# Performance work log

Measured on AMD Instinct MI355X. Metric: run time of the kernel, lower is better.

## Reference

```python
import jax, jax.numpy as jnp
import numpy as np

N_NODES = 100000
N_PART = 5000
N_EDGES = 1000000
D_NODE = 128
D_PART = 128
D_ATT = 20


def setup_inputs() -> dict:
    key = jax.random.key(0)
    ks = jax.random.split(key, 20)
    inp = {
        "nodes_hidden": jax.random.normal(ks[0], (N_NODES, D_NODE), jnp.float32),
        "particles_hidden": jax.random.normal(ks[1], (N_PART, D_PART), jnp.float32),
        "global_rep": jax.random.normal(ks[2], (N_PART, D_NODE), jnp.float32),
        "src": jax.random.randint(ks[3], (N_EDGES,), 0, N_NODES, jnp.int32),
        "dst": jax.random.randint(ks[4], (N_EDGES,), 0, N_PART, jnp.int32),
        "key_W": jax.random.normal(ks[5], (D_NODE, D_ATT), jnp.float32) * 0.05,
        "key_b": jnp.zeros((D_ATT,), jnp.float32),
        "val_W": jax.random.normal(ks[6], (D_NODE, D_PART), jnp.float32) * 0.05,
        "val_b": jnp.zeros((D_PART,), jnp.float32),
        "q_W": jax.random.normal(ks[7], (D_PART + D_NODE, D_ATT), jnp.float32) * 0.05,
        "q_b": jnp.zeros((D_ATT,), jnp.float32),
        "W_ih": jax.random.normal(ks[8], (3 * D_PART, D_PART), jnp.float32) * 0.05,
        "W_hh": jax.random.normal(ks[9], (3 * D_PART, D_PART), jnp.float32) * 0.05,
        "b_ih": jnp.zeros((3 * D_PART,), jnp.float32),
        "b_hh": jnp.zeros((3 * D_PART,), jnp.float32),
        "ln_g": jnp.ones((D_PART,), jnp.float32),
        "ln_b": jnp.zeros((D_PART,), jnp.float32),
        "mlp_W1": jax.random.normal(ks[10], (D_PART, 64), jnp.float32) * 0.05,
        "mlp_b1": jnp.zeros((64,), jnp.float32),
        "mlp_W2": jax.random.normal(ks[11], (64, D_PART), jnp.float32) * 0.05,
        "mlp_b2": jnp.zeros((D_PART,), jnp.float32),
    }
    return inp


def reference(nodes_hidden, particles_hidden, global_rep, src, dst,
              key_W, key_b, val_W, val_b, q_W, q_b,
              W_ih, W_hh, b_ih, b_hh, ln_g, ln_b,
              mlp_W1, mlp_b1, mlp_W2, mlp_b2):
    norm = jnp.float32(1.0) / jnp.sqrt(jnp.float32(D_ATT))
    keys = nodes_hidden @ key_W + key_b          # [N, 20]
    vals = nodes_hidden @ val_W + val_b          # [N, P]
    q_in = jnp.concatenate([particles_hidden, global_rep], axis=1)
    query = q_in @ q_W + q_b                     # [Np, 20]

    # per-edge raw attention (ReLU'd copy in edges.data is unused downstream)
    att = jnp.sum(keys[src] * query[dst], axis=1) * norm     # [E]
    msg = att[:, None] * vals[src]                            # [E, P]
    weighted_sum = jax.ops.segment_sum(msg, dst, num_segments=particles_hidden.shape[0])

    # GRUCell(input=weighted_sum, hidden=particles_hidden), torch semantics
    gi = weighted_sum @ W_ih.T + b_ih
    gh = particles_hidden @ W_hh.T + b_hh
    i_r, i_z, i_n = jnp.split(gi, 3, axis=1)
    h_r, h_z, h_n = jnp.split(gh, 3, axis=1)
    r = jax.nn.sigmoid(i_r + h_r)
    z = jax.nn.sigmoid(i_z + h_z)
    n = jnp.tanh(i_n + r * h_n)
    h_new = (1.0 - z) * n + z * particles_hidden

    # LayerNorm (eps=1e-5)
    mu = jnp.mean(h_new, axis=-1, keepdims=True)
    var = jnp.mean(jnp.square(h_new - mu), axis=-1, keepdims=True)
    ln = (h_new - mu) * jax.lax.rsqrt(var + 1e-5) * ln_g + ln_b

    mlp_out = jax.nn.relu(ln @ mlp_W1 + mlp_b1) @ mlp_W2 + mlp_b2
    return particles_hidden + mlp_out
```

## Files before the change

kernel.cpp:

```cpp
#include <hip/hip_runtime.h>
#include <math.h>

#define N_NODES 100000
#define N_PART  5000
#define N_EDGES 1000000
#define D_NODE  128
#define D_PART  128
#define D_ATT   20
#define NBLK    128
#define EPB     ((N_EDGES + NBLK - 1) / NBLK)
#define TPV6    8

__device__ __forceinline__ float sigmoid_(float x) { return 1.f / (1.f + __expf(-x)); }
__device__ __forceinline__ float tanh_(float x)    { return 1.f - 2.f / (__expf(2.f * x) + 1.f); }

__global__ __launch_bounds__(256) void build_wbig_kernel(
    const float* __restrict__ valW, const float* __restrict__ Wih,
    const float* __restrict__ Whh, float* __restrict__ Wbig)
{
    int idx = blockIdx.x * 256 + threadIdx.x;
    int k = idx >> 9;
    int jn = idx & 511;
    int j = (jn & 3) * 128 + (jn >> 2);
    float v = 0.f;
    if (k < 128) {
        if (j < 384) {
            float acc = 0.f;
            #pragma unroll 8
            for (int m = 0; m < 128; m++)
                acc += valW[k * 128 + m] * Wih[j * 128 + m];
            v = acc;
        }
    } else {
        int kp = k - 128;
        if (j < 256)       v = Whh[j * 128 + kp];
        else if (j >= 384) v = Whh[(j - 128) * 128 + kp];
    }
    Wbig[k * 512 + jn] = v;
}

__global__ __launch_bounds__(256) void build_bvec_kernel(
    const float* __restrict__ valb, const float* __restrict__ Wih,
    float* __restrict__ bvec)
{
    int c = blockIdx.x * 256 + threadIdx.x;
    if (c < 384) {
        float acc = 0.f;
        #pragma unroll 8
        for (int m = 0; m < 128; m++) acc += valb[m] * Wih[c * 128 + m];
        bvec[c] = acc;
    }
}

__global__ __launch_bounds__(128) void query_qk_kernel(
    const float* __restrict__ ph, const float* __restrict__ gr,
    const float* __restrict__ qW, const float* __restrict__ qb,
    const float* __restrict__ keyW, const float* __restrict__ keyb,
    float* __restrict__ qk, float* __restrict__ qoff)
{
    int p = blockIdx.x;
    int t = threadIdx.x;
    __shared__ float s_in[256];
    __shared__ float s_q[D_ATT];

    s_in[t]       = ph[p * 128 + t];
    s_in[128 + t] = gr[p * 128 + t];
    __syncthreads();

    if (t < D_ATT) {
        float acc = qb[t];
        #pragma unroll 8
        for (int k = 0; k < 256; k++) acc += s_in[k] * qW[k * D_ATT + t];
        s_q[t] = acc;
    }
    __syncthreads();

    float acc = 0.f;
    #pragma unroll
    for (int a = 0; a < D_ATT; a++) acc += keyW[t * D_ATT + a] * s_q[a];
    qk[p * 128 + t] = acc;

    if (t == 0) {
        float o = 0.f;
        #pragma unroll
        for (int a = 0; a < D_ATT; a++) o += keyb[a] * s_q[a];
        qoff[p] = o;
    }
}

__global__ __launch_bounds__(256) void block_hist_kernel(
    const int* __restrict__ dst, int* __restrict__ blockhist)
{
    __shared__ int h[N_PART];
    int b = blockIdx.x;
    for (int i = threadIdx.x; i < N_PART; i += 256) h[i] = 0;
    __syncthreads();
    int beg = b * EPB, end = min(beg + EPB, N_EDGES);
    for (int e = beg + threadIdx.x; e < end; e += 256)
        atomicAdd(&h[dst[e]], 1);
    __syncthreads();
    for (int i = threadIdx.x; i < N_PART; i += 256)
        blockhist[(size_t)b * N_PART + i] = h[i];
}

__global__ __launch_bounds__(256) void colscan_kernel(
    int* __restrict__ blockhist, int* __restrict__ totals)
{
    int i = blockIdx.x * 256 + threadIdx.x;
    if (i >= N_PART) return;
    int run = 0;
    for (int b = 0; b < NBLK; b++) {
        size_t idx = (size_t)b * N_PART + i;
        int v = blockhist[idx];
        blockhist[idx] = run;
        run += v;
    }
    totals[i] = run;
}

__global__ __launch_bounds__(256) void scan_kernel(
    const int* __restrict__ totals, int* __restrict__ offsets)
{
    __shared__ int ss[256];
    int t = threadIdx.x;
    const int CH = 20;
    int beg = t * CH;
    int end = min(beg + CH, N_PART);
    int lsum = 0;
    for (int i = beg; i < end; i++) lsum += totals[i];
    ss[t] = lsum;
    __syncthreads();
    for (int off = 1; off < 256; off <<= 1) {
        int v = (t >= off) ? ss[t - off] : 0;
        __syncthreads();
        ss[t] += v;
        __syncthreads();
    }
    int base = ss[t] - lsum;
    for (int i = beg; i < end; i++) {
        offsets[i] = base;
        base += totals[i];
    }
    if (t == 0) offsets[N_PART] = N_EDGES;
}

__global__ __launch_bounds__(256) void scatter_sorted_kernel(
    const int* __restrict__ src, const int* __restrict__ dst,
    const int* __restrict__ offsets, const int* __restrict__ blockhist,
    int* __restrict__ ssrc)
{
    __shared__ int cur[N_PART];
    int b = blockIdx.x;
    for (int i = threadIdx.x; i < N_PART; i += 256)
        cur[i] = offsets[i] + blockhist[(size_t)b * N_PART + i];
    __syncthreads();
    int beg = b * EPB, end = min(beg + EPB, N_EDGES);
    for (int e = beg + threadIdx.x; e < end; e += 256) {
        int d = dst[e];
        int pos = atomicAdd(&cur[d], 1);
        ssrc[pos] = src[e];
    }
}

__global__ __launch_bounds__(256) void edge_agg_kernel(
    const float* __restrict__ nodes, const float* __restrict__ qk,
    const float* __restrict__ qoff,
    const int* __restrict__ offsets, const int* __restrict__ ssrc,
    float* __restrict__ agg, float* __restrict__ att_sum)
{
    const float norm = 0.22360679774997896f;
    int p = blockIdx.x;
    int tid = threadIdx.x;
    int lane = tid & 63;
    int wave = tid >> 6;
    int half = lane >> 5;
    int colq = (lane & 31) * 4;

    const float4 q = *(const float4*)(qk + (size_t)p * 128 + colq);
    float qo = qoff[p];
    int beg = offsets[p], end = offsets[p + 1];
    int n = end - beg;
    int np = (n + 1) >> 1;
    int npfull = n >> 1;

    float4 a = {0.f, 0.f, 0.f, 0.f};
    float asum = 0.f;

    int pi = wave;
    for (; pi + 12 < npfull; pi += 16) {
        int e0 = beg + 2 * pi + half;
        int s0 = ssrc[e0];
        int s1 = ssrc[e0 + 8];
        int s2 = ssrc[e0 + 16];
        int s3 = ssrc[e0 + 24];
        float4 x0 = *(const float4*)(nodes + (size_t)s0 * 128 + colq);
        float4 x1 = *(const float4*)(nodes + (size_t)s1 * 128 + colq);
        float4 x2 = *(const float4*)(nodes + (size_t)s2 * 128 + colq);
        float4 x3 = *(const float4*)(nodes + (size_t)s3 * 128 + colq);
        float d0 = x0.x * q.x + x0.y * q.y + x0.z * q.z + x0.w * q.w;
        float d1 = x1.x * q.x + x1.y * q.y + x1.z * q.z + x1.w * q.w;
        float d2 = x2.x * q.x + x2.y * q.y + x2.z * q.z + x2.w * q.w;
        float d3 = x3.x * q.x + x3.y * q.y + x3.z * q.z + x3.w * q.w;
        #pragma unroll
        for (int off = 1; off <= 16; off <<= 1) {
            d0 += __shfl_xor(d0, off, 64);
            d1 += __shfl_xor(d1, off, 64);
            d2 += __shfl_xor(d2, off, 64);
            d3 += __shfl_xor(d3, off, 64);
        }
        float t0 = (d0 + qo) * norm;
        float t1 = (d1 + qo) * norm;
        float t2 = (d2 + qo) * norm;
        float t3 = (d3 + qo) * norm;
        a.x += t0 * x0.x + t1 * x1.x + t2 * x2.x + t3 * x3.x;
        a.y += t0 * x0.y + t1 * x1.y + t2 * x2.y + t3 * x3.y;
        a.z += t0 * x0.z + t1 * x1.z + t2 * x2.z + t3 * x3.z;
        a.w += t0 * x0.w + t1 * x1.w + t2 * x2.w + t3 * x3.w;
        asum += t0 + t1 + t2 + t3;
    }
    for (; pi < np; pi += 4) {
        int e0 = beg + 2 * pi;
        bool has1 = (e0 + 1 < end);
        int s0 = ssrc[e0];
        int s1 = has1 ? ssrc[e0 + 1] : s0;
        int s = half ? s1 : s0;
        float4 x = *(const float4*)(nodes + (size_t)s * 128 + colq);
        float d = x.x * q.x + x.y * q.y + x.z * q.z + x.w * q.w;
        #pragma unroll
        for (int off = 1; off <= 16; off <<= 1) d += __shfl_xor(d, off, 64);
        float att = (d + qo) * norm;
        if (half && !has1) att = 0.f;
        a.x += att * x.x; a.y += att * x.y; a.z += att * x.z; a.w += att * x.w;
        asum += att;
    }

    a.x += __shfl_xor(a.x, 32, 64);
    a.y += __shfl_xor(a.y, 32, 64);
    a.z += __shfl_xor(a.z, 32, 64);
    a.w += __shfl_xor(a.w, 32, 64);
    asum += __shfl_xor(asum, 32, 64);

    __shared__ float s_acc[4][128];
    __shared__ float s_as[4];
    if (lane < 32) {
        *(float4*)&s_acc[wave][colq] = a;
        if (lane == 0) s_as[wave] = asum;
    }
    __syncthreads();

    if (tid < 128) {
        float v = s_acc[0][tid] + s_acc[1][tid] + s_acc[2][tid] + s_acc[3][tid];
        agg[(size_t)p * 128 + tid] = v;
        if (tid == 0) att_sum[p] = s_as[0] + s_as[1] + s_as[2] + s_as[3];
    }
}

__global__ __launch_bounds__(256) void gru_fused_v6(
    const float* __restrict__ agg, const float* __restrict__ att_sum,
    const float* __restrict__ ph,
    const float* __restrict__ Wbig, const float* __restrict__ bvec,
    const float* __restrict__ bih, const float* __restrict__ bhh,
    const float* __restrict__ lng, const float* __restrict__ lnb,
    const float* __restrict__ W1, const float* __restrict__ b1,
    const float* __restrict__ W2, const float* __restrict__ b2,
    float* __restrict__ out)
{
    __shared__ float s_in[TPV6][256];
    __shared__ float s_ln[TPV6][128];
    __shared__ float s_hid[TPV6][64];

    int t = threadIdx.x;
    int pbase = blockIdx.x * TPV6;

    for (int f = t; f < TPV6 * 64; f += 256) {
        int pl = f >> 6, r = f & 63;
        int c4 = r * 4;
        int p = pbase + pl;
        float4 v;
        if (c4 < 128) v = *(const float4*)(agg + (size_t)p * 128 + c4);
        else          v = *(const float4*)(ph + (size_t)p * 128 + (c4 - 128));
        *(float4*)&s_in[pl][c4] = v;
    }

    int c  = t & 127;
    int j4 = c * 4;
    int pg = t >> 7;
    float4 cb, bv;
    cb.x = bih[c]       + bhh[c];        bv.x = bvec[c];
    cb.y = bih[128 + c] + bhh[128 + c];  bv.y = bvec[128 + c];
    cb.z = bih[256 + c];                 bv.z = bvec[256 + c];
    cb.w = bhh[256 + c];                 bv.w = 0.f;
    float4 acc[4];
    #pragma unroll
    for (int i = 0; i < 4; i++) {
        float as = att_sum[pbase + pg * 4 + i];
        acc[i].x = cb.x + as * bv.x;
        acc[i].y = cb.y + as * bv.y;
        acc[i].z = cb.z + as * bv.z;
        acc[i].w = cb.w + as * bv.w;
    }
    __syncthreads();

    const float* wp = Wbig + j4;
    float4 w0 = *(const float4*)(wp);
    float4 w1 = *(const float4*)(wp + 512);
    float4 w2 = *(const float4*)(wp + 1024);
    float4 w3 = *(const float4*)(wp + 1536);
    float4 x0 = *(const float4*)&s_in[pg * 4 + 0][0];
    float4 x1 = *(const float4*)&s_in[pg * 4 + 1][0];
    float4 x2 = *(const float4*)&s_in[pg * 4 + 2][0];
    float4 x3 = *(const float4*)&s_in[pg * 4 + 3][0];
    for (int k = 0; k < 256; k += 4) {
        float4 cw0 = w0, cw1 = w1, cw2 = w2, cw3 = w3;
        float4 cx0 = x0, cx1 = x1, cx2 = x2, cx3 = x3;
        if (k < 252) {
            const float* wn = wp + (size_t)(k + 4) * 512;
            w0 = *(const float4*)(wn);
            w1 = *(const float4*)(wn + 512);
            w2 = *(const float4*)(wn + 1024);
            w3 = *(const float4*)(wn + 1536);
            x0 = *(const float4*)&s_in[pg * 4 + 0][k + 4];
            x1 = *(const float4*)&s_in[pg * 4 + 1][k + 4];
            x2 = *(const float4*)&s_in[pg * 4 + 2][k + 4];
            x3 = *(const float4*)&s_in[pg * 4 + 3][k + 4];
        }
        acc[0].x += cx0.x * cw0.x + cx0.y * cw1.x + cx0.z * cw2.x + cx0.w * cw3.x;
        acc[0].y += cx0.x * cw0.y + cx0.y * cw1.y + cx0.z * cw2.y + cx0.w * cw3.y;
        acc[0].z += cx0.x * cw0.z + cx0.y * cw1.z + cx0.z * cw2.z + cx0.w * cw3.z;
        acc[0].w += cx0.x * cw0.w + cx0.y * cw1.w + cx0.z * cw2.w + cx0.w * cw3.w;
        acc[1].x += cx1.x * cw0.x + cx1.y * cw1.x + cx1.z * cw2.x + cx1.w * cw3.x;
        acc[1].y += cx1.x * cw0.y + cx1.y * cw1.y + cx1.z * cw2.y + cx1.w * cw3.y;
        acc[1].z += cx1.x * cw0.z + cx1.y * cw1.z + cx1.z * cw2.z + cx1.w * cw3.z;
        acc[1].w += cx1.x * cw0.w + cx1.y * cw1.w + cx1.z * cw2.w + cx1.w * cw3.w;
        acc[2].x += cx2.x * cw0.x + cx2.y * cw1.x + cx2.z * cw2.x + cx2.w * cw3.x;
        acc[2].y += cx2.x * cw0.y + cx2.y * cw1.y + cx2.z * cw2.y + cx2.w * cw3.y;
        acc[2].z += cx2.x * cw0.z + cx2.y * cw1.z + cx2.z * cw2.z + cx2.w * cw3.z;
        acc[2].w += cx2.x * cw0.w + cx2.y * cw1.w + cx2.z * cw2.w + cx2.w * cw3.w;
        acc[3].x += cx3.x * cw0.x + cx3.y * cw1.x + cx3.z * cw2.x + cx3.w * cw3.x;
        acc[3].y += cx3.x * cw0.y + cx3.y * cw1.y + cx3.z * cw2.y + cx3.w * cw3.y;
        acc[3].z += cx3.x * cw0.z + cx3.y * cw1.z + cx3.z * cw2.z + cx3.w * cw3.z;
        acc[3].w += cx3.x * cw0.w + cx3.y * cw1.w + cx3.z * cw2.w + cx3.w * cw3.w;
    }

    #pragma unroll
    for (int i = 0; i < 4; i++) {
        int pl = pg * 4 + i;
        float r = sigmoid_(acc[i].x);
        float z = sigmoid_(acc[i].y);
        float n = tanh_(acc[i].z + r * acc[i].w);
        float h = s_in[pl][128 + c];
        s_ln[pl][c] = (1.f - z) * n + z * h;
    }
    __syncthreads();

    {
        int wv = t >> 6, l = t & 63;
        for (int pl = wv; pl < TPV6; pl += 4) {
            float v0 = s_ln[pl][l * 2], v1 = s_ln[pl][l * 2 + 1];
            float sum = v0 + v1, sq = v0 * v0 + v1 * v1;
            #pragma unroll
            for (int off = 1; off <= 32; off <<= 1) {
                sum += __shfl_xor(sum, off, 64);
                sq  += __shfl_xor(sq, off, 64);
            }
            float mu = sum * (1.f / 128.f);
            float var = sq * (1.f / 128.f) - mu * mu;
            float rstd = rsqrtf(var + 1e-5f);
            s_ln[pl][l * 2]     = (v0 - mu) * rstd * lng[l * 2] + lnb[l * 2];
            s_ln[pl][l * 2 + 1] = (v1 - mu) * rstd * lng[l * 2 + 1] + lnb[l * 2 + 1];
        }
    }
    __syncthreads();

    for (int idx = t; idx < TPV6 * 64; idx += 256) {
        int pl = idx >> 6, u = idx & 63;
        float a0 = b1[u];
        #pragma unroll 4
        for (int k = 0; k < 128; k++) a0 += s_ln[pl][k] * W1[k * 64 + u];
        s_hid[pl][u] = fmaxf(a0, 0.f);
    }
    __syncthreads();

    for (int idx = t; idx < TPV6 * 32; idx += 256) {
        int pl = idx >> 5, qd = idx & 31;
        int c4 = qd * 4;
        float4 o = *(const float4*)(b2 + c4);
        #pragma unroll 4
        for (int u = 0; u < 64; u++) {
            float av = s_hid[pl][u];
            float4 w = *(const float4*)(W2 + u * 128 + c4);
            o.x += av * w.x; o.y += av * w.y; o.z += av * w.z; o.w += av * w.w;
        }
        float4 h4 = *(const float4*)&s_in[pl][128 + c4];
        float4 res;
        res.x = h4.x + o.x; res.y = h4.y + o.y;
        res.z = h4.z + o.z; res.w = h4.w + o.w;
        *(float4*)(out + (size_t)(pbase + pl) * 128 + c4) = res;
    }
}

extern "C" void kernel_launch(void* const* d_in, const int* in_sizes, int n_in,
                              void* d_out, int out_size, void* d_ws, size_t ws_size,
                              hipStream_t stream) {
    const float* nodes = (const float*)d_in[0];
    const float* ph    = (const float*)d_in[1];
    const float* gr    = (const float*)d_in[2];
    const int*   src   = (const int*)d_in[3];
    const int*   dst   = (const int*)d_in[4];
    const float* keyW  = (const float*)d_in[5];
    const float* keyb  = (const float*)d_in[6];
    const float* valW  = (const float*)d_in[7];
    const float* valb  = (const float*)d_in[8];
    const float* qW    = (const float*)d_in[9];
    const float* qb    = (const float*)d_in[10];
    const float* Wih   = (const float*)d_in[11];
    const float* Whh   = (const float*)d_in[12];
    const float* bih   = (const float*)d_in[13];
    const float* bhh   = (const float*)d_in[14];
    const float* lng   = (const float*)d_in[15];
    const float* lnb   = (const float*)d_in[16];
    const float* W1    = (const float*)d_in[17];
    const float* b1    = (const float*)d_in[18];
    const float* W2    = (const float*)d_in[19];
    const float* b2    = (const float*)d_in[20];
    float* out = (float*)d_out;

    float* ws_f      = (float*)d_ws;
    float* qk        = ws_f;
    float* qoff      = qk + 640000;
    float* agg       = qoff + 5008;
    float* att_sum   = agg + 640000;
    int*   totals    = (int*)(att_sum + 5008);
    int*   offsets   = totals + 5008;
    int*   blockhist = offsets + 5008;
    int*   ssrc      = blockhist + (size_t)NBLK * N_PART;
    float* Wbig      = (float*)(ssrc + 1000000);
    float* bvec      = Wbig + 131072;

    build_wbig_kernel<<<512, 256, 0, stream>>>(valW, Wih, Whh, Wbig);
    build_bvec_kernel<<<2, 256, 0, stream>>>(valb, Wih, bvec);
    query_qk_kernel<<<N_PART, 128, 0, stream>>>(ph, gr, qW, qb, keyW, keyb, qk, qoff);
    block_hist_kernel<<<NBLK, 256, 0, stream>>>(dst, blockhist);
    colscan_kernel<<<(N_PART + 255) / 256, 256, 0, stream>>>(blockhist, totals);
    scan_kernel<<<1, 256, 0, stream>>>(totals, offsets);
    scatter_sorted_kernel<<<NBLK, 256, 0, stream>>>(src, dst, offsets, blockhist, ssrc);
    edge_agg_kernel<<<N_PART, 256, 0, stream>>>(nodes, qk, qoff, offsets, ssrc, agg, att_sum);
    gru_fused_v6<<<N_PART / TPV6, 256, 0, stream>>>(
        agg, att_sum, ph, Wbig, bvec, bih, bhh, lng, lnb, W1, b1, W2, b2, out);
}
```

Baseline: 307.3 us.

## Fold query and key weights into one matrix and batch the query GEMM

Precomputes Wq = qW·keyWᵀ plus bias terms in a small setup kernel, so qk becomes one 256x128 GEMM per particle. That GEMM runs in a batched kernel handling 8 particles per block with float4 register prefetch, replacing the one-block-per-particle two-stage reduction. The GRU GEMM loop is also restructured into two interleaved prefetch streams to raise memory-level parallelism. This adds a 32K-element weight build and more register pressure.

```diff
diff --git a/kernel.cpp b/kernel.cpp
--- a/kernel.cpp
+++ b/kernel.cpp
@@ -13,6 +13,37 @@
 
 __device__ __forceinline__ float sigmoid_(float x) { return 1.f / (1.f + __expf(-x)); }
 __device__ __forceinline__ float tanh_(float x)    { return 1.f - 2.f / (__expf(2.f * x) + 1.f); }
+
+__device__ __forceinline__ void gru_body(float4 acc[4],
+    float4 w0, float4 w1, float4 w2, float4 w3,
+    float4 x0, float4 x1, float4 x2, float4 x3)
+{
+    acc[0].x += x0.x * w0.x + x0.y * w1.x + x0.z * w2.x + x0.w * w3.x;
+    acc[0].y += x0.x * w0.y + x0.y * w1.y + x0.z * w2.y + x0.w * w3.y;
+    acc[0].z += x0.x * w0.z + x0.y * w1.z + x0.z * w2.z + x0.w * w3.z;
+    acc[0].w += x0.x * w0.w + x0.y * w1.w + x0.z * w2.w + x0.w * w3.w;
+    acc[1].x += x1.x * w0.x + x1.y * w1.x + x1.z * w2.x + x1.w * w3.x;
+    acc[1].y += x1.x * w0.y + x1.y * w1.y + x1.z * w2.y + x1.w * w3.y;
+    acc[1].z += x1.x * w0.z + x1.y * w1.z + x1.z * w2.z + x1.w * w3.z;
+    acc[1].w += x1.x * w0.w + x1.y * w1.w + x1.z * w2.w + x1.w * w3.w;
+    acc[2].x += x2.x * w0.x + x2.y * w1.x + x2.z * w2.x + x2.w * w3.x;
+    acc[2].y += x2.x * w0.y + x2.y * w1.y + x2.z * w2.y + x2.w * w3.y;
+    acc[2].z += x2.x * w0.z + x2.y * w1.z + x2.z * w2.z + x2.w * w3.z;
+    acc[2].w += x2.x * w0.w + x2.y * w1.w + x2.z * w2.w + x2.w * w3.w;
+    acc[3].x += x3.x * w0.x + x3.y * w1.x + x3.z * w2.x + x3.w * w3.x;
+    acc[3].y += x3.x * w0.y + x3.y * w1.y + x3.z * w2.y + x3.w * w3.y;
+    acc[3].z += x3.x * w0.z + x3.y * w1.z + x3.z * w2.z + x3.w * w3.z;
+    acc[3].w += x3.x * w0.w + x3.y * w1.w + x3.z * w2.w + x3.w * w3.w;
+}
+
+__device__ __forceinline__ void q_body(float4& acc,
+    float4 w0, float4 w1, float4 w2, float4 w3, float4 x)
+{
+    acc.x += x.x * w0.x + x.y * w1.x + x.z * w2.x + x.w * w3.x;
+    acc.y += x.x * w0.y + x.y * w1.y + x.z * w2.y + x.w * w3.y;
+    acc.z += x.x * w0.z + x.y * w1.z + x.z * w2.z + x.w * w3.z;
+    acc.w += x.x * w0.w + x.y * w1.w + x.z * w2.w + x.w * w3.w;
+}
 
 __global__ __launch_bounds__(256) void build_wbig_kernel(
     const float* __restrict__ valW, const float* __restrict__ Wih,
@@ -39,12 +70,40 @@
     Wbig[k * 512 + jn] = v;
 }
 
-__global__ __launch_bounds__(256) void build_bvec_kernel(
+__global__ __launch_bounds__(256) void build_small_kernel(
+    const float* __restrict__ qW, const float* __restrict__ qb,
+    const float* __restrict__ keyW, const float* __restrict__ keyb,
     const float* __restrict__ valb, const float* __restrict__ Wih,
+    float* __restrict__ Wq, float* __restrict__ qoffW,
+    float* __restrict__ cqk, float* __restrict__ cqoff,
     float* __restrict__ bvec)
 {
-    int c = blockIdx.x * 256 + threadIdx.x;
-    if (c < 384) {
+    int jx = blockIdx.x * 256 + threadIdx.x;
+    if (jx < 32768) {
+        int k = jx >> 7, j = jx & 127;
+        float acc = 0.f;
+        #pragma unroll
+        for (int a = 0; a < D_ATT; a++) acc += qW[k * D_ATT + a] * keyW[j * D_ATT + a];
+        Wq[k * 128 + j] = acc;
+    } else if (jx < 33024) {
+        int k = jx - 32768;
+        float acc = 0.f;
+        #pragma unroll
+        for (int a = 0; a < D_ATT; a++) acc += qW[k * D_ATT + a] * keyb[a];
+        qoffW[k] = acc;
+    } else if (jx < 33152) {
+        int j = jx - 33024;
+        float acc = 0.f;
+        #pragma unroll
+        for (int a = 0; a < D_ATT; a++) acc += keyW[j * D_ATT + a] * qb[a];
+        cqk[j] = acc;
+    } else if (jx == 33152) {
+        float acc = 0.f;
+        #pragma unroll
+        for (int a = 0; a < D_ATT; a++) acc += keyb[a] * qb[a];
+        cqoff[0] = acc;
+    } else if (jx >= 33280 && jx < 33664) {
+        int c = jx - 33280;
         float acc = 0.f;
         #pragma unroll 8
         for (int m = 0; m < 128; m++) acc += valb[m] * Wih[c * 128 + m];
@@ -52,39 +111,84 @@
     }
 }
 
-__global__ __launch_bounds__(128) void query_qk_kernel(
+__global__ __launch_bounds__(256) void query_gemm_kernel(
     const float* __restrict__ ph, const float* __restrict__ gr,
-    const float* __restrict__ qW, const float* __restrict__ qb,
-    const float* __restrict__ keyW, const float* __restrict__ keyb,
+    const float* __restrict__ Wq, const float* __restrict__ qoffW,
+    const float* __restrict__ cqk, const float* __restrict__ cqoff,
     float* __restrict__ qk, float* __restrict__ qoff)
 {
-    int p = blockIdx.x;
+    __shared__ float s_in[TPV6][256];
     int t = threadIdx.x;
-    __shared__ float s_in[256];
-    __shared__ float s_q[D_ATT];
-
-    s_in[t]       = ph[p * 128 + t];
-    s_in[128 + t] = gr[p * 128 + t];
-    __syncthreads();
-
-    if (t < D_ATT) {
-        float acc = qb[t];
-        #pragma unroll 8
-        for (int k = 0; k < 256; k++) acc += s_in[k] * qW[k * D_ATT + t];
-        s_q[t] = acc;
-    }
-    __syncthreads();
-
-    float acc = 0.f;
+    int pbase = blockIdx.x * TPV6;
+
+    for (int f = t; f < TPV6 * 64; f += 256) {
+        int pl = f >> 6, r = f & 63;
+        int c4 = r * 4;
+        int p = pbase + pl;
+        float4 v;
+        if (c4 < 128) v = *(const float4*)(ph + (size_t)p * 128 + c4);
+        else          v = *(const float4*)(gr + (size_t)p * 128 + (c4 - 128));
+        *(float4*)&s_in[pl][c4] = v;
+    }
+    __syncthreads();
+
+    int cq = (t & 31) * 4;
+    int pl = t >> 5;
+    const float* wp = Wq + cq;
+
+    float4 acc = {0.f, 0.f, 0.f, 0.f};
+    float4 wa0 = *(const float4*)(wp);
+    float4 wa1 = *(const float4*)(wp + 128);
+    float4 wa2 = *(const float4*)(wp + 256);
+    float4 wa3 = *(const float4*)(wp + 384);
+    float4 xa  = *(const float4*)&s_in[pl][0];
+    float4 wb0 = *(const float4*)(wp + 512);
+    float4 wb1 = *(const float4*)(wp + 640);
+    float4 wb2 = *(const float4*)(wp + 768);
+    float4 wb3 = *(const float4*)(wp + 896);
+    float4 xb  = *(const float4*)&s_in[pl][4];
+
+    for (int k = 0; k < 256; k += 8) {
+        float4 ca0 = wa0, ca1 = wa1, ca2 = wa2, ca3 = wa3, cxa = xa;
+        if (k + 8 < 256) {
+            const float* wn = wp + (size_t)(k + 8) * 128;
+            wa0 = *(const float4*)(wn);
+            wa1 = *(const float4*)(wn + 128);
+            wa2 = *(const float4*)(wn + 256);
+            wa3 = *(const float4*)(wn + 384);
+            xa  = *(const float4*)&s_in[pl][k + 8];
+        }
+        q_body(acc, ca0, ca1, ca2, ca3, cxa);
+        float4 cb0 = wb0, cb1 = wb1, cb2 = wb2, cb3 = wb3, cxb = xb;
+        if (k + 12 < 256) {
+            const float* wn = wp + (size_t)(k + 12) * 128;
+            wb0 = *(const float4*)(wn);
+            wb1 = *(const float4*)(wn + 128);
+            wb2 = *(const float4*)(wn + 256);
+            wb3 = *(const float4*)(wn + 384);
+            xb  = *(const float4*)&s_in[pl][k + 12];
+        }
+        q_body(acc, cb0, cb1, cb2, cb3, cxb);
+    }
+
+    float4 cst = *(const float4*)(cqk + cq);
+    float4 o;
+    o.x = cst.x + acc.x; o.y = cst.y + acc.y;
+    o.z = cst.z + acc.z; o.w = cst.w + acc.w;
+    *(float4*)(qk + (size_t)(pbase + pl) * 128 + cq) = o;
+
+    int wv = t >> 6, l = t & 63;
+    float co = cqoff[0];
     #pragma unroll
-    for (int a = 0; a < D_ATT; a++) acc += keyW[t * D_ATT + a] * s_q[a];
-    qk[p * 128 + t] = acc;
-
-    if (t == 0) {
-        float o = 0.f;
-        #pragma unroll
-        for (int a = 0; a < D_ATT; a++) o += keyb[a] * s_q[a];
-        qoff[p] = o;
+    for (int i = 0; i < 2; i++) {
+        int pp = wv * 2 + i;
+        float s = s_in[pp][l]       * qoffW[l]
+                + s_in[pp][l + 64]  * qoffW[l + 64]
+                + s_in[pp][l + 128] * qoffW[l + 128]
+                + s_in[pp][l + 192] * qoffW[l + 192];
+        #pragma unroll
+        for (int off = 1; off <= 32; off <<= 1) s += __shfl_xor(s, off, 64);
+        if (l == 0) qoff[pbase + pp] = co + s;
     }
 }
 
@@ -255,7 +359,7 @@
     }
 }
 
-__global__ __launch_bounds__(256) void gru_fused_v6(
+__global__ __launch_bounds__(256) void gru_fused_v7(
     const float* __restrict__ agg, const float* __restrict__ att_sum,
     const float* __restrict__ ph,
     const float* __restrict__ Wbig, const float* __restrict__ bvec,
@@ -302,44 +406,52 @@
     __syncthreads();
 
     const float* wp = Wbig + j4;
-    float4 w0 = *(const float4*)(wp);
-    float4 w1 = *(const float4*)(wp + 512);
-    float4 w2 = *(const float4*)(wp + 1024);
-    float4 w3 = *(const float4*)(wp + 1536);
-    float4 x0 = *(const float4*)&s_in[pg * 4 + 0][0];
-    float4 x1 = *(const float4*)&s_in[pg * 4 + 1][0];
-    float4 x2 = *(const float4*)&s_in[pg * 4 + 2][0];
-    float4 x3 = *(const float4*)&s_in[pg * 4 + 3][0];
-    for (int k = 0; k < 256; k += 4) {
-        float4 cw0 = w0, cw1 = w1, cw2 = w2, cw3 = w3;
-        float4 cx0 = x0, cx1 = x1, cx2 = x2, cx3 = x3;
-        if (k < 252) {
-            const float* wn = wp + (size_t)(k + 4) * 512;
-            w0 = *(const float4*)(wn);
-            w1 = *(const float4*)(wn + 512);
-            w2 = *(const float4*)(wn + 1024);
-            w3 = *(const float4*)(wn + 1536);
-            x0 = *(const float4*)&s_in[pg * 4 + 0][k + 4];
-            x1 = *(const float4*)&s_in[pg * 4 + 1][k + 4];
-            x2 = *(const float4*)&s_in[pg * 4 + 2][k + 4];
-            x3 = *(const float4*)&s_in[pg * 4 + 3][k + 4];
-        }
-        acc[0].x += cx0.x * cw0.x + cx0.y * cw1.x + cx0.z * cw2.x + cx0.w * cw3.x;
-        acc[0].y += cx0.x * cw0.y + cx0.y * cw1.y + cx0.z * cw2.y + cx0.w * cw3.y;
-        acc[0].z += cx0.x * cw0.z + cx0.y * cw1.z + cx0.z * cw2.z + cx0.w * cw3.z;
-        acc[0].w += cx0.x * cw0.w + cx0.y * cw1.w + cx0.z * cw2.w + cx0.w * cw3.w;
-        acc[1].x += cx1.x * cw0.x + cx1.y * cw1.x + cx1.z * cw2.x + cx1.w * cw3.x;
-        acc[1].y += cx1.x * cw0.y + cx1.y * cw1.y + cx1.z * cw2.y + cx1.w * cw3.y;
-        acc[1].z += cx1.x * cw0.z + cx1.y * cw1.z + cx1.z * cw2.z + cx1.w * cw3.z;
-        acc[1].w += cx1.x * cw0.w + cx1.y * cw1.w + cx1.z * cw2.w + cx1.w * cw3.w;
-        acc[2].x += cx2.x * cw0.x + cx2.y * cw1.x + cx2.z * cw2.x + cx2.w * cw3.x;
-        acc[2].y += cx2.x * cw0.y + cx2.y * cw1.y + cx2.z * cw2.y + cx2.w * cw3.y;
-        acc[2].z += cx2.x * cw0.z + cx2.y * cw1.z + cx2.z * cw2.z + cx2.w * cw3.z;
-        acc[2].w += cx2.x * cw0.w + cx2.y * cw1.w + cx2.z * cw2.w + cx2.w * cw3.w;
-        acc[3].x += cx3.x * cw0.x + cx3.y * cw1.x + cx3.z * cw2.x + cx3.w * cw3.x;
-        acc[3].y += cx3.x * cw0.y + cx3.y * cw1.y + cx3.z * cw2.y + cx3.w * cw3.y;
-        acc[3].z += cx3.x * cw0.z + cx3.y * cw1.z + cx3.z * cw2.z + cx3.w * cw3.z;
-        acc[3].w += cx3.x * cw0.w + cx3.y * cw1.w + cx3.z * cw2.w + cx3.w * cw3.w;
+    float4 wa0 = *(const float4*)(wp);
+    float4 wa1 = *(const float4*)(wp + 512);
+    float4 wa2 = *(const float4*)(wp + 1024);
+    float4 wa3 = *(const float4*)(wp + 1536);
+    float4 xa0 = *(const float4*)&s_in[pg * 4 + 0][0];
+    float4 xa1 = *(const float4*)&s_in[pg * 4 + 1][0];
+    float4 xa2 = *(const float4*)&s_in[pg * 4 + 2][0];
+    float4 xa3 = *(const float4*)&s_in[pg * 4 + 3][0];
+    float4 wb0 = *(const float4*)(wp + 2048);
+    float4 wb1 = *(const float4*)(wp + 2560);
+    float4 wb2 = *(const float4*)(wp + 3072);
+    float4 wb3 = *(const float4*)(wp + 3584);
+    float4 xb0 = *(const float4*)&s_in[pg * 4 + 0][4];
+    float4 xb1 = *(const float4*)&s_in[pg * 4 + 1][4];
+    float4 xb2 = *(const float4*)&s_in[pg * 4 + 2][4];
+    float4 xb3 = *(const float4*)&s_in[pg * 4 + 3][4];
+
+    for (int k = 0; k < 256; k += 8) {
+        float4 ca0 = wa0, ca1 = wa1, ca2 = wa2, ca3 = wa3;
+        float4 cx0 = xa0, cx1 = xa1, cx2 = xa2, cx3 = xa3;
+        if (k + 8 < 256) {
+            const float* wn = wp + (size_t)(k + 8) * 512;
+            wa0 = *(const float4*)(wn);
+            wa1 = *(const float4*)(wn + 512);
+            wa2 = *(const float4*)(wn + 1024);
+            wa3 = *(const float4*)(wn + 1536);
+            xa0 = *(const float4*)&s_in[pg * 4 + 0][k + 8];
+            xa1 = *(const float4*)&s_in[pg * 4 + 1][k + 8];
+            xa2 = *(const float4*)&s_in[pg * 4 + 2][k + 8];
+            xa3 = *(const float4*)&s_in[pg * 4 + 3][k + 8];
+        }
+        gru_body(acc, ca0, ca1, ca2, ca3, cx0, cx1, cx2, cx3);
+        float4 cb0 = wb0, cb1 = wb1, cb2 = wb2, cb3 = wb3;
+        float4 dx0 = xb0, dx1 = xb1, dx2 = xb2, dx3 = xb3;
+        if (k + 12 < 256) {
+            const float* wn = wp + (size_t)(k + 12) * 512;
+            wb0 = *(const float4*)(wn);
+            wb1 = *(const float4*)(wn + 512);
+            wb2 = *(const float4*)(wn + 1024);
+            wb3 = *(const float4*)(wn + 1536);
+            xb0 = *(const float4*)&s_in[pg * 4 + 0][k + 12];
+            xb1 = *(const float4*)&s_in[pg * 4 + 1][k + 12];
+            xb2 = *(const float4*)&s_in[pg * 4 + 2][k + 12];
+            xb3 = *(const float4*)&s_in[pg * 4 + 3][k + 12];
+        }
+        gru_body(acc, cb0, cb1, cb2, cb3, dx0, dx1, dx2, dx3);
     }
 
     #pragma unroll
@@ -436,15 +548,21 @@
     int*   ssrc      = blockhist + (size_t)NBLK * N_PART;
     float* Wbig      = (float*)(ssrc + 1000000);
     float* bvec      = Wbig + 131072;
+    float* Wq        = bvec + 512;
+    float* qoffW     = Wq + 32768;
+    float* cqk       = qoffW + 256;
+    float* cqoff     = cqk + 128;
 
     build_wbig_kernel<<<512, 256, 0, stream>>>(valW, Wih, Whh, Wbig);
-    build_bvec_kernel<<<2, 256, 0, stream>>>(valb, Wih, bvec);
-    query_qk_kernel<<<N_PART, 128, 0, stream>>>(ph, gr, qW, qb, keyW, keyb, qk, qoff);
+    build_small_kernel<<<132, 256, 0, stream>>>(qW, qb, keyW, keyb, valb, Wih,
+                                                Wq, qoffW, cqk, cqoff, bvec);
+    query_gemm_kernel<<<N_PART / TPV6, 256, 0, stream>>>(
+        ph, gr, Wq, qoffW, cqk, cqoff, qk, qoff);
     block_hist_kernel<<<NBLK, 256, 0, stream>>>(dst, blockhist);
     colscan_kernel<<<(N_PART + 255) / 256, 256, 0, stream>>>(blockhist, totals);
     scan_kernel<<<1, 256, 0, stream>>>(totals, offsets);
     scatter_sorted_kernel<<<NBLK, 256, 0, stream>>>(src, dst, offsets, blockhist, ssrc);
     edge_agg_kernel<<<N_PART, 256, 0, stream>>>(nodes, qk, qoff, offsets, ssrc, agg, att_sum);
-    gru_fused_v6<<<N_PART / TPV6, 256, 0, stream>>>(
+    gru_fused_v7<<<N_PART / TPV6, 256, 0, stream>>>(
         agg, att_sum, ph, Wbig, bvec, bih, bhh, lng, lnb, W1, b1, W2, b2, out);
 }
```

Result: slower. 319.6 us (+4.0%).

## Fuse weight prep, histogram and query kernels into one multi-role launch

Applied to the files above, without the earlier changes.

Four independent front-end kernels (Wbig build, bias build, per-block dst histogram, query/qk projection) are merged into one launch whose blocks branch by block index. The query part now handles 8 particles per block, with keyW staged in shared memory and vectorized stores, instead of one block per particle. This cuts three kernel launches and lets the independent jobs overlap on the GPU. In exchange every block reserves 20KB of shared memory, which can lower occupancy for the roles that need none. The GRU inner loop is also pulled out into a helper function, which is cleanup only.

```diff
diff --git a/kernel.cpp b/kernel.cpp
--- a/kernel.cpp
+++ b/kernel.cpp
@@ -10,97 +10,144 @@
 #define NBLK    128
 #define EPB     ((N_EDGES + NBLK - 1) / NBLK)
 #define TPV6    8
+#define QBLKS   (N_PART / TPV6)
 
 __device__ __forceinline__ float sigmoid_(float x) { return 1.f / (1.f + __expf(-x)); }
 __device__ __forceinline__ float tanh_(float x)    { return 1.f - 2.f / (__expf(2.f * x) + 1.f); }
 
-__global__ __launch_bounds__(256) void build_wbig_kernel(
+__device__ __forceinline__ void gru_body(float4 acc[4],
+    float4 w0, float4 w1, float4 w2, float4 w3,
+    float4 x0, float4 x1, float4 x2, float4 x3)
+{
+    acc[0].x += x0.x * w0.x + x0.y * w1.x + x0.z * w2.x + x0.w * w3.x;
+    acc[0].y += x0.x * w0.y + x0.y * w1.y + x0.z * w2.y + x0.w * w3.y;
+    acc[0].z += x0.x * w0.z + x0.y * w1.z + x0.z * w2.z + x0.w * w3.z;
+    acc[0].w += x0.x * w0.w + x0.y * w1.w + x0.z * w2.w + x0.w * w3.w;
+    acc[1].x += x1.x * w0.x + x1.y * w1.x + x1.z * w2.x + x1.w * w3.x;
+    acc[1].y += x1.x * w0.y + x1.y * w1.y + x1.z * w2.y + x1.w * w3.y;
+    acc[1].z += x1.x * w0.z + x1.y * w1.z + x1.z * w2.z + x1.w * w3.z;
+    acc[1].w += x1.x * w0.w + x1.y * w1.w + x1.z * w2.w + x1.w * w3.w;
+    acc[2].x += x2.x * w0.x + x2.y * w1.x + x2.z * w2.x + x2.w * w3.x;
+    acc[2].y += x2.x * w0.y + x2.y * w1.y + x2.z * w2.y + x2.w * w3.y;
+    acc[2].z += x2.x * w0.z + x2.y * w1.z + x2.z * w2.z + x2.w * w3.z;
+    acc[2].w += x2.x * w0.w + x2.y * w1.w + x2.z * w2.w + x2.w * w3.w;
+    acc[3].x += x3.x * w0.x + x3.y * w1.x + x3.z * w2.x + x3.w * w3.x;
+    acc[3].y += x3.x * w0.y + x3.y * w1.y + x3.z * w2.y + x3.w * w3.y;
+    acc[3].z += x3.x * w0.z + x3.y * w1.z + x3.z * w2.z + x3.w * w3.z;
+    acc[3].w += x3.x * w0.w + x3.y * w1.w + x3.z * w2.w + x3.w * w3.w;
+}
+
+__global__ __launch_bounds__(256) void fused_front_kernel(
     const float* __restrict__ valW, const float* __restrict__ Wih,
-    const float* __restrict__ Whh, float* __restrict__ Wbig)
-{
-    int idx = blockIdx.x * 256 + threadIdx.x;
-    int k = idx >> 9;
-    int jn = idx & 511;
-    int j = (jn & 3) * 128 + (jn >> 2);
-    float v = 0.f;
-    if (k < 128) {
-        if (j < 384) {
-            float acc = 0.f;
-            #pragma unroll 8
-            for (int m = 0; m < 128; m++)
-                acc += valW[k * 128 + m] * Wih[j * 128 + m];
-            v = acc;
-        }
-    } else {
-        int kp = k - 128;
-        if (j < 256)       v = Whh[j * 128 + kp];
-        else if (j >= 384) v = Whh[(j - 128) * 128 + kp];
-    }
-    Wbig[k * 512 + jn] = v;
-}
-
-__global__ __launch_bounds__(256) void build_bvec_kernel(
-    const float* __restrict__ valb, const float* __restrict__ Wih,
-    float* __restrict__ bvec)
-{
-    int c = blockIdx.x * 256 + threadIdx.x;
-    if (c < 384) {
-        float acc = 0.f;
-        #pragma unroll 8
-        for (int m = 0; m < 128; m++) acc += valb[m] * Wih[c * 128 + m];
-        bvec[c] = acc;
-    }
-}
-
-__global__ __launch_bounds__(128) void query_qk_kernel(
+    const float* __restrict__ Whh, float* __restrict__ Wbig,
+    const float* __restrict__ valb, float* __restrict__ bvec,
+    const int* __restrict__ dst, int* __restrict__ blockhist,
     const float* __restrict__ ph, const float* __restrict__ gr,
     const float* __restrict__ qW, const float* __restrict__ qb,
     const float* __restrict__ keyW, const float* __restrict__ keyb,
     float* __restrict__ qk, float* __restrict__ qoff)
 {
-    int p = blockIdx.x;
+    __shared__ float pool[5000];
+    int blk = blockIdx.x;
     int t = threadIdx.x;
-    __shared__ float s_in[256];
-    __shared__ float s_q[D_ATT];
-
-    s_in[t]       = ph[p * 128 + t];
-    s_in[128 + t] = gr[p * 128 + t];
-    __syncthreads();
-
-    if (t < D_ATT) {
-        float acc = qb[t];
-        #pragma unroll 8
-        for (int k = 0; k < 256; k++) acc += s_in[k] * qW[k * D_ATT + t];
-        s_q[t] = acc;
-    }
-    __syncthreads();
-
-    float acc = 0.f;
-    #pragma unroll
-    for (int a = 0; a < D_ATT; a++) acc += keyW[t * D_ATT + a] * s_q[a];
-    qk[p * 128 + t] = acc;
-
-    if (t == 0) {
-        float o = 0.f;
-        #pragma unroll
-        for (int a = 0; a < D_ATT; a++) o += keyb[a] * s_q[a];
-        qoff[p] = o;
-    }
-}
-
-__global__ __launch_bounds__(256) void block_hist_kernel(
-    const int* __restrict__ dst, int* __restrict__ blockhist)
-{
-    __shared__ int h[N_PART];
-    int b = blockIdx.x;
-    for (int i = threadIdx.x; i < N_PART; i += 256) h[i] = 0;
-    __syncthreads();
-    int beg = b * EPB, end = min(beg + EPB, N_EDGES);
-    for (int e = beg + threadIdx.x; e < end; e += 256)
-        atomicAdd(&h[dst[e]], 1);
-    __syncthreads();
-    for (int i = threadIdx.x; i < N_PART; i += 256)
-        blockhist[(size_t)b * N_PART + i] = h[i];
+
+    if (blk < 512) {
+        int idx = blk * 256 + t;
+        int k = idx >> 9;
+        int jn = idx & 511;
+        int j = (jn & 3) * 128 + (jn >> 2);
+        float v = 0.f;
+        if (k < 128) {
+            if (j < 384) {
+                float acc = 0.f;
+                #pragma unroll 8
+                for (int m = 0; m < 128; m++)
+                    acc += valW[k * 128 + m] * Wih[j * 128 + m];
+                v = acc;
+            }
+        } else {
+            int kp = k - 128;
+            if (j < 256)       v = Whh[j * 128 + kp];
+            else if (j >= 384) v = Whh[(j - 128) * 128 + kp];
+        }
+        Wbig[k * 512 + jn] = v;
+    } else if (blk < 514) {
+        int c = (blk - 512) * 256 + t;
+        if (c < 384) {
+            float acc = 0.f;
+            #pragma unroll 8
+            for (int m = 0; m < 128; m++) acc += valb[m] * Wih[c * 128 + m];
+            bvec[c] = acc;
+        }
+    } else if (blk < 642) {
+        int b = blk - 514;
+        int* h = (int*)pool;
+        for (int i = t; i < N_PART; i += 256) h[i] = 0;
+        __syncthreads();
+        int beg = b * EPB, end = min(beg + EPB, N_EDGES);
+        for (int e = beg + t; e < end; e += 256)
+            atomicAdd(&h[dst[e]], 1);
+        __syncthreads();
+        for (int i = t; i < N_PART; i += 256)
+            blockhist[(size_t)b * N_PART + i] = h[i];
+    } else {
+        float (*s_in)[260] = (float (*)[260])pool;
+        float (*s_q)[20]   = (float (*)[20])(pool + 2080);
+        float (*s_kw)[21]  = (float (*)[21])(pool + 2240);
+        float* s_kb = pool + 4928;
+        float* s_qb = pool + 4948;
+
+        int pbase = (blk - 642) * TPV6;
+
+        for (int f = t; f < TPV6 * 64; f += 256) {
+            int pl = f >> 6, r = f & 63;
+            int c4 = r * 4;
+            int p = pbase + pl;
+            float4 v;
+            if (c4 < 128) v = *(const float4*)(ph + (size_t)p * 128 + c4);
+            else          v = *(const float4*)(gr + (size_t)p * 128 + (c4 - 128));
+            *(float4*)&s_in[pl][c4] = v;
+        }
+        for (int f = t; f < 2560; f += 256) {
+            int j = f / 20, a = f - j * 20;
+            s_kw[j][a] = keyW[f];
+        }
+        if (t < 20) { s_kb[t] = keyb[t]; s_qb[t] = qb[t]; }
+        __syncthreads();
+
+        if (t < 160) {
+            int pl = t / 20, a = t - (t / 20) * 20;
+            float acc = s_qb[a];
+            const float* qwp = qW + a;
+            #pragma unroll 8
+            for (int k = 0; k < 256; k++) acc += s_in[pl][k] * qwp[k * 20];
+            s_q[pl][a] = acc;
+        }
+        __syncthreads();
+
+        {
+            int pl = t >> 5, j0 = (t & 31) * 4;
+            float4 o;
+            float acc0 = 0.f, acc1 = 0.f, acc2 = 0.f, acc3 = 0.f;
+            #pragma unroll
+            for (int a = 0; a < 20; a++) {
+                float qv = s_q[pl][a];
+                acc0 += qv * s_kw[j0][a];
+                acc1 += qv * s_kw[j0 + 1][a];
+                acc2 += qv * s_kw[j0 + 2][a];
+                acc3 += qv * s_kw[j0 + 3][a];
+            }
+            o.x = acc0; o.y = acc1; o.z = acc2; o.w = acc3;
+            *(float4*)(qk + (size_t)(pbase + pl) * 128 + j0) = o;
+
+            if (t < TPV6) {
+                float acc = 0.f;
+                #pragma unroll
+                for (int a = 0; a < 20; a++) acc += s_kb[a] * s_q[t][a];
+                qoff[pbase + t] = acc;
+            }
+        }
+    }
 }
 
 __global__ __launch_bounds__(256) void colscan_kernel(
@@ -324,22 +371,7 @@
             x2 = *(const float4*)&s_in[pg * 4 + 2][k + 4];
             x3 = *(const float4*)&s_in[pg * 4 + 3][k + 4];
         }
-        acc[0].x += cx0.x * cw0.x + cx0.y * cw1.x + cx0.z * cw2.x + cx0.w * cw3.x;
-        acc[0].y += cx0.x * cw0.y + cx0.y * cw1.y + cx0.z * cw2.y + cx0.w * cw3.y;
-        acc[0].z += cx0.x * cw0.z + cx0.y * cw1.z + cx0.z * cw2.z + cx0.w * cw3.z;
-        acc[0].w += cx0.x * cw0.w + cx0.y * cw1.w + cx0.z * cw2.w + cx0.w * cw3.w;
-        acc[1].x += cx1.x * cw0.x + cx1.y * cw1.x + cx1.z * cw2.x + cx1.w * cw3.x;
-        acc[1].y += cx1.x * cw0.y + cx1.y * cw1.y + cx1.z * cw2.y + cx1.w * cw3.y;
-        acc[1].z += cx1.x * cw0.z + cx1.y * cw1.z + cx1.z * cw2.z + cx1.w * cw3.z;
-        acc[1].w += cx1.x * cw0.w + cx1.y * cw1.w + cx1.z * cw2.w + cx1.w * cw3.w;
-        acc[2].x += cx2.x * cw0.x + cx2.y * cw1.x + cx2.z * cw2.x + cx2.w * cw3.x;
-        acc[2].y += cx2.x * cw0.y + cx2.y * cw1.y + cx2.z * cw2.y + cx2.w * cw3.y;
-        acc[2].z += cx2.x * cw0.z + cx2.y * cw1.z + cx2.z * cw2.z + cx2.w * cw3.z;
-        acc[2].w += cx2.x * cw0.w + cx2.y * cw1.w + cx2.z * cw2.w + cx2.w * cw3.w;
-        acc[3].x += cx3.x * cw0.x + cx3.y * cw1.x + cx3.z * cw2.x + cx3.w * cw3.x;
-        acc[3].y += cx3.x * cw0.y + cx3.y * cw1.y + cx3.z * cw2.y + cx3.w * cw3.y;
-        acc[3].z += cx3.x * cw0.z + cx3.y * cw1.z + cx3.z * cw2.z + cx3.w * cw3.z;
-        acc[3].w += cx3.x * cw0.w + cx3.y * cw1.w + cx3.z * cw2.w + cx3.w * cw3.w;
+        gru_body(acc, cw0, cw1, cw2, cw3, cx0, cx1, cx2, cx3);
     }
 
     #pragma unroll
@@ -437,14 +469,20 @@
     float* Wbig      = (float*)(ssrc + 1000000);
     float* bvec      = Wbig + 131072;
 
-    build_wbig_kernel<<<512, 256, 0, stream>>>(valW, Wih, Whh, Wbig);
-    build_bvec_kernel<<<2, 256, 0, stream>>>(valb, Wih, bvec);
-    query_qk_kernel<<<N_PART, 128, 0, stream>>>(ph, gr, qW, qb, keyW, keyb, qk, qoff);
-    block_hist_kernel<<<NBLK, 256, 0, stream>>>(dst, blockhist);
+    fused_front_kernel<<<512 + 2 + NBLK + QBLKS, 256, 0, stream>>>(
+        valW, Wih, Whh, Wbig,
+        valb, bvec,
+        dst, blockhist,
+        ph, gr, qW, qb, keyW, keyb, qk, qoff);
+
     colscan_kernel<<<(N_PART + 255) / 256, 256, 0, stream>>>(blockhist, totals);
+
     scan_kernel<<<1, 256, 0, stream>>>(totals, offsets);
+
     scatter_sorted_kernel<<<NBLK, 256, 0, stream>>>(src, dst, offsets, blockhist, ssrc);
+
     edge_agg_kernel<<<N_PART, 256, 0, stream>>>(nodes, qk, qoff, offsets, ssrc, agg, att_sum);
+
     gru_fused_v6<<<N_PART / TPV6, 256, 0, stream>>>(
         agg, att_sum, ph, Wbig, bvec, bih, bhh, lng, lnb, W1, b1, W2, b2, out);
 }
```

Measured after the change: 280.6 us. 1.09x faster.
